# Kernel optimization log

Hardware: AMD Instinct MI355X
Metric: run time of the kernel (lower is better)

The kernel has to match this reference:

```python
import jax, jax.numpy as jnp
import numpy as np

D_MODEL = 512
NHEAD = 8
HEAD_DIM = D_MODEL // NHEAD  # 64
ROTARY_DIM = HEAD_DIM        # rotary_dim defaults to head_dim
WINDOW = (127, 128)          # (left, right) sliding window, flash-attn convention
ROPE_BASE = 10000.0


def setup_inputs() -> dict:
    key = jax.random.key(0)
    k1, k2, k3, k4 = jax.random.split(key, 4)
    N, T = 4, 2048
    x = jax.random.normal(k1, (N, T, D_MODEL), dtype=jnp.float32)
    # Wqkv: Linear(d_model, 3*d_model, bias=False) -> weight [3*D, D]
    Wqkv_w = jax.random.normal(k2, (3 * D_MODEL, D_MODEL), dtype=jnp.float32) * (D_MODEL ** -0.5)
    # out_proj: Linear(d_model, d_model, bias=True)
    out_w = jax.random.normal(k3, (D_MODEL, D_MODEL), dtype=jnp.float32) * (D_MODEL ** -0.5)
    out_b = jax.random.normal(k4, (D_MODEL,), dtype=jnp.float32) * 0.01
    return {"x": x, "Wqkv_w": Wqkv_w, "out_w": out_w, "out_b": out_b}


def _rope_cos_sin(T, dtype):
    # flash-attn RotaryEmbedding: inv_freq over even indices of rotary_dim
    inv_freq = 1.0 / (ROPE_BASE ** (jnp.arange(0, ROTARY_DIM, 2, dtype=jnp.float32) / ROTARY_DIM))
    t = jnp.arange(T, dtype=jnp.float32)
    freqs = jnp.outer(t, inv_freq)  # [T, ROTARY_DIM//2]
    return jnp.cos(freqs).astype(dtype), jnp.sin(freqs).astype(dtype)


def _apply_rotary(x, cos, sin):
    # non-interleaved (rotate halves); x: [N, T, H, hd], rotary over first ROTARY_DIM dims
    r, rest = x[..., :ROTARY_DIM], x[..., ROTARY_DIM:]
    half = ROTARY_DIM // 2
    x1, x2 = r[..., :half], r[..., half:]
    c = cos[None, :, None, :]  # [1, T, 1, half]
    s = sin[None, :, None, :]
    rotated = jnp.concatenate([x1 * c - x2 * s, x2 * c + x1 * s], axis=-1)
    return jnp.concatenate([rotated, rest], axis=-1) if rest.shape[-1] else rotated


def reference(x, Wqkv_w, out_w, out_b):
    N, T, D = x.shape
    qkv = jnp.einsum('ntd,ed->nte', x, Wqkv_w).reshape(N, T, 3, NHEAD, HEAD_DIM)
    q, k, v = qkv[:, :, 0], qkv[:, :, 1], qkv[:, :, 2]  # each [N, T, H, hd]
    cos, sin = _rope_cos_sin(T, x.dtype)
    q = _apply_rotary(q, cos, sin)
    k = _apply_rotary(k, cos, sin)
    scale = HEAD_DIM ** -0.5
    scores = jnp.einsum('nthd,nshd->nhts', q, k) * scale  # [N, H, T, T]
    # sliding window: query i attends key j iff i - left <= j <= i + right
    i = jnp.arange(T)[:, None]
    j = jnp.arange(T)[None, :]
    mask = (j >= i - WINDOW[0]) & (j <= i + WINDOW[1])  # [T, T]
    scores = jnp.where(mask[None, None], scores, jnp.finfo(scores.dtype).min)
    attn = jax.nn.softmax(scores, axis=-1)
    ctx = jnp.einsum('nhts,nshd->nthd', attn, v).reshape(N, T, D)
    return jnp.einsum('ntd,ed->nte', ctx, out_w) + out_b
```

## Files before the change

kernel.cpp:

```cpp
#include <hip/hip_runtime.h>
#include <math.h>

#define TSEQ 2048
#define NB 4
#define DM 512
#define NH 8
#define HD 64

typedef _Float16 half8 __attribute__((ext_vector_type(8)));
typedef _Float16 half4 __attribute__((ext_vector_type(4)));
typedef float floatx4 __attribute__((ext_vector_type(4)));

#if __has_builtin(__builtin_amdgcn_exp2f)
#define EXP2F(x) __builtin_amdgcn_exp2f(x)
#else
#define EXP2F(x) exp2f(x)
#endif

__device__ __forceinline__ void gl2lds16(const _Float16* g, _Float16* l) {
  const __attribute__((address_space(1))) unsigned int* gp =
      (const __attribute__((address_space(1))) unsigned int*)(uintptr_t)g;
  __attribute__((address_space(3))) unsigned int* lp =
      (__attribute__((address_space(3))) unsigned int*)(uintptr_t)l;
  __builtin_amdgcn_global_load_lds(gp, lp, 16, 0, 0);
}


__device__ __forceinline__ void cvt8(const float* __restrict__ src, char* __restrict__ dst,
                                     int unit_src, int unit_dst) {
  const float4 a = ((const float4*)src)[2 * unit_src];
  const float4 b = ((const float4*)src)[2 * unit_src + 1];
  half8 h;
  h[0] = (_Float16)a.x; h[1] = (_Float16)a.y; h[2] = (_Float16)a.z; h[3] = (_Float16)a.w;
  h[4] = (_Float16)b.x; h[5] = (_Float16)b.y; h[6] = (_Float16)b.z; h[7] = (_Float16)b.w;
  *(half8*)(dst + (size_t)unit_dst * 16) = h;
}

__global__ void prep(const float* __restrict__ x, const float* __restrict__ wqkv,
                     const float* __restrict__ ow, char* __restrict__ ws) {
  const int i = blockIdx.x * 256 + threadIdx.x;
  if (i < 524288) {
    cvt8(x, ws, i, i);
  } else if (i < 622592) {
    const int o = i - 524288;
    cvt8(wqkv, ws + 8650752, o, o);
  } else if (i < 655360) {
    const int o = i - 622592;
    cvt8(ow, ws + 10485760, o, o);
  } else {
    const int u = i - 655360;
    float4 o4;
    {
      const int id = 2 * u, t = id >> 5, fi = id & 31;
      const float invf = powf(10000.0f, -(float)(2 * fi) * (1.0f / 64.0f));
      float s, c; sincosf((float)t * invf, &s, &c);
      o4.x = c; o4.y = s;
    }
    {
      const int id = 2 * u + 1, t = id >> 5, fi = id & 31;
      const float invf = powf(10000.0f, -(float)(2 * fi) * (1.0f / 64.0f));
      float s, c; sincosf((float)t * invf, &s, &c);
      o4.z = c; o4.w = s;
    }
    ((float4*)(ws + 46137344))[u] = o4;
  }
}

__global__ __launch_bounds__(256) void qkv_gemm_mfma(
    const _Float16* __restrict__ A, const _Float16* __restrict__ B,
    const float2* __restrict__ rope,
    _Float16* __restrict__ qb, _Float16* __restrict__ kb, _Float16* __restrict__ vT)
{
  __shared__ __align__(16) _Float16 As0[128 * 32];
  __shared__ __align__(16) _Float16 Bs0[128 * 32];
  __shared__ __align__(16) _Float16 As1[128 * 32];
  __shared__ __align__(16) _Float16 Bs1[128 * 32];
  const int tid = threadIdx.x;
  const int wv = tid >> 6, lane = tid & 63, quad = lane >> 4, col = lane & 15;
  const int wm = wv >> 1, we = wv & 1;
  const int m0 = blockIdx.x << 7, c0 = blockIdx.y << 7;
  const int r0 = tid >> 2, p0 = tid & 3;
  const int cA0 = (p0 - (r0 >> 1)) & 3;
  const int r1 = (tid + 256) >> 2, p1 = tid & 3;
  const int cA1 = (p1 - (r1 >> 1)) & 3;
  const _Float16* ga0 = &A[(size_t)(m0 + r0) * DM + cA0 * 8];
  const _Float16* ga1 = &A[(size_t)(m0 + r1) * DM + cA1 * 8];
  const _Float16* gb0 = &B[(size_t)(c0 + r0) * DM + cA0 * 8];
  const _Float16* gb1 = &B[(size_t)(c0 + r1) * DM + cA1 * 8];
  floatx4 acc[4][4] = {};

#define QKV_STAGE(AS, BS, K)                      \
  do {                                            \
    gl2lds16(ga0 + (K), &AS[tid * 8]);            \
    gl2lds16(ga1 + (K), &AS[(tid + 256) * 8]);    \
    gl2lds16(gb0 + (K), &BS[tid * 8]);            \
    gl2lds16(gb1 + (K), &BS[(tid + 256) * 8]);    \
  } while (0)

#define QKV_COMPUTE(AS, BS)                                                   \
  do {                                                                        \
    half8 af[4], bf[4];                                                       \
    _Pragma("unroll") for (int mt = 0; mt < 4; mt++) {                        \
      const int R = wm * 64 + mt * 16 + col;                                  \
      af[mt] = *(const half8*)&AS[R * 32 + (((quad + (R >> 1)) & 3) << 3)];   \
    }                                                                         \
    _Pragma("unroll") for (int et = 0; et < 4; et++) {                        \
      const int R = we * 64 + et * 16 + col;                                  \
      bf[et] = *(const half8*)&BS[R * 32 + (((quad + (R >> 1)) & 3) << 3)];   \
    }                                                                         \
    _Pragma("unroll") for (int mt = 0; mt < 4; mt++)                          \
      _Pragma("unroll") for (int et = 0; et < 4; et++)                        \
        acc[mt][et] =                                                         \
            __builtin_amdgcn_mfma_f32_16x16x32_f16(af[mt], bf[et], acc[mt][et], 0, 0, 0); \
  } while (0)

  QKV_STAGE(As0, Bs0, 0);
  for (int k0 = 0; k0 < DM; k0 += 64) {
    __syncthreads();
    QKV_STAGE(As1, Bs1, k0 + 32);
    QKV_COMPUTE(As0, Bs0);
    __syncthreads();
    if (k0 + 64 < DM) QKV_STAGE(As0, Bs0, k0 + 64);
    QKV_COMPUTE(As1, Bs1);
  }
#undef QKV_STAGE
#undef QKV_COMPUTE

  const int eidx = (c0 >> 6) + we;
  const int three = eidx >> 3, h = eidx & 7;
  const int mbase = m0 + wm * 64 + quad * 4;
  if (three == 2) {
#pragma unroll
    for (int mt = 0; mt < 4; mt++) {
      const int m = mbase + mt * 16;
      const int n = m >> 11, t = m & 2047;
#pragma unroll
      for (int et = 0; et < 4; et++) {
        const int dh = et * 16 + col;
        half4 hv;
#pragma unroll
        for (int r = 0; r < 4; r++) hv[r] = (_Float16)acc[mt][et][r];
        *(half4*)&vT[(size_t)(n * NH + h) * HD * TSEQ + (size_t)dh * TSEQ + t] = hv;
      }
    }
  } else {
    _Float16* dst = three ? kb : qb;
    const float scl = three ? 1.0f : 0.125f * 1.4426950408889634f;
#pragma unroll
    for (int mt = 0; mt < 4; mt++)
#pragma unroll
      for (int r = 0; r < 4; r++) {
        const int m = mbase + mt * 16 + r;
        const int n = m >> 11, t = m & 2047;
#pragma unroll
        for (int et = 0; et < 4; et++) {
          const int i = ((et & 1) << 4) + col;
          const float2 cs = rope[t * 32 + i];
          const float v = acc[mt][et][r];
          const float v2 = acc[mt][et ^ 2][r];
          const float o = (et < 2) ? (v * cs.x - v2 * cs.y) : (v * cs.x + v2 * cs.y);
          dst[((size_t)(n * NH + h) * TSEQ + t) * HD + et * 16 + col] = (_Float16)(o * scl);
        }
      }
  }
}

__global__ __launch_bounds__(256, 4) void attn_win_mfma(
    const _Float16* __restrict__ qb, const _Float16* __restrict__ kb,
    const _Float16* __restrict__ vT, _Float16* __restrict__ ctx)
{
  __shared__ __align__(16) char smem[36864];
  _Float16* Ks = (_Float16*)smem;
  _Float16* Vt = (_Float16*)(smem + 9216);
  _Float16* Ps = (_Float16*)(smem + 18432);
  _Float16* Osh = (_Float16*)(smem + 27648);

  const int tid = threadIdx.x;
  const int wv = tid >> 6;
  const int lane = tid & 63;
  const int quad = lane >> 4;
  const int col = lane & 15;
  const int lin = (blockIdx.y << 5) | blockIdx.x;
  const int sl  = ((lin & 7) << 7) | (lin >> 3);
  const int nh = sl >> 5;
  const int q0 = (sl & 31) << 6;
  const _Float16* qp = qb + (size_t)nh * TSEQ * HD;
  const _Float16* kp = kb + (size_t)nh * TSEQ * HD;
  const _Float16* vp = vT + (size_t)nh * HD * TSEQ;

  const int i_row = (wv << 4) + col;
  const int ig = q0 + i_row;
  const half8 qf0 = *(const half8*)&qp[(size_t)ig * HD + (quad << 3)];
  const half8 qf1 = *(const half8*)&qp[(size_t)ig * HD + 32 + (quad << 3)];

  float l_i = 0.0f;
  floatx4 accO[4] = {};

  const int kt0 = max(0, q0 - 127) >> 6;
  const int kt1 = min(TSEQ - 1, q0 + 191) >> 6;
  const int kr = tid >> 2, kc = (tid & 3) << 4;
  const int vd = tid >> 2, vc = (tid & 3) << 4;
  const _Float16* kpr = kp + (size_t)kr * HD + kc;
  const _Float16* vpr = vp + (size_t)vd * TSEQ + vc;

  half8 ck0 = *(const half8*)(kpr + (size_t)(kt0 << 6) * HD);
  half8 ck1 = *(const half8*)(kpr + (size_t)(kt0 << 6) * HD + 8);
  half8 cv0 = *(const half8*)(vpr + (kt0 << 6));
  half8 cv1 = *(const half8*)(vpr + (kt0 << 6) + 8);

  for (int kt = kt0; kt <= kt1; kt++) {
    const int j0 = kt << 6;
    __syncthreads();
    *(half8*)&Ks[kr * 72 + kc] = ck0;
    *(half8*)&Ks[kr * 72 + kc + 8] = ck1;
    *(half8*)&Vt[vd * 72 + vc] = cv0;
    *(half8*)&Vt[vd * 72 + vc + 8] = cv1;
    __syncthreads();

    {
      const int jn = (kt < kt1) ? (j0 + 64) : j0;
      ck0 = *(const half8*)(kpr + (size_t)jn * HD);
      ck1 = *(const half8*)(kpr + (size_t)jn * HD + 8);
      cv0 = *(const half8*)(vpr + jn);
      cv1 = *(const half8*)(vpr + jn + 8);
    }

    floatx4 S[4];
#pragma unroll
    for (int js = 0; js < 4; js++) {
      const half8 a0 = *(const half8*)&Ks[((js << 4) + col) * 72 + (quad << 3)];
      const half8 a1 = *(const half8*)&Ks[((js << 4) + col) * 72 + 32 + (quad << 3)];
      floatx4 c = {0.f, 0.f, 0.f, 0.f};
      c = __builtin_amdgcn_mfma_f32_16x16x32_f16(a0, qf0, c, 0, 0, 0);
      c = __builtin_amdgcn_mfma_f32_16x16x32_f16(a1, qf1, c, 0, 0, 0);
      S[js] = c;
    }
    const int relb = j0 - ig + 127 + (quad << 2);
#pragma unroll
    for (int js = 0; js < 4; js++) {
      half4 ph;
#pragma unroll
      for (int r = 0; r < 4; r++) {
        const bool valid = (unsigned)(relb + (js << 4) + r) < 256u;
        const float p = valid ? EXP2F(S[js][r]) : 0.0f;
        l_i += p;
        ph[r] = (_Float16)p;
      }
      *(half4*)&Ps[i_row * 72 + (js << 4) + (quad << 2)] = ph;
    }
    const half8 pa0 = *(const half8*)&Ps[i_row * 72 + (quad << 3)];
    const half8 pa1 = *(const half8*)&Ps[i_row * 72 + 32 + (quad << 3)];
#pragma unroll
    for (int d4 = 0; d4 < 4; d4++) {
      const half8 vb0 = *(const half8*)&Vt[((d4 << 4) + col) * 72 + (quad << 3)];
      const half8 vb1 = *(const half8*)&Vt[((d4 << 4) + col) * 72 + 32 + (quad << 3)];
      accO[d4] = __builtin_amdgcn_mfma_f32_16x16x32_f16(pa0, vb0, accO[d4], 0, 0, 0);
      accO[d4] = __builtin_amdgcn_mfma_f32_16x16x32_f16(pa1, vb1, accO[d4], 0, 0, 0);
    }
  }
  l_i += __shfl_xor(l_i, 16, 64);
  l_i += __shfl_xor(l_i, 32, 64);
  {
    const float linv = 1.0f / l_i;
    float l4[4];
#pragma unroll
    for (int r = 0; r < 4; r++) l4[r] = __shfl(linv, (quad << 2) + r, 64);
#pragma unroll
    for (int d4 = 0; d4 < 4; d4++)
#pragma unroll
      for (int r = 0; r < 4; r++)
        Osh[((wv << 4) + (quad << 2) + r) * 72 + (d4 << 4) + col] = (_Float16)(accO[d4][r] * l4[r]);
  }
  __syncthreads();
  {
    const int n = nh >> 3, h = nh & 7;
    const int oi = tid >> 2, oc = (tid & 3) << 4;
    _Float16* dst = &ctx[((size_t)n * TSEQ + q0 + oi) * DM + h * HD + oc];
    *(half8*)&dst[0] = *(const half8*)&Osh[oi * 72 + oc];
    *(half8*)&dst[8] = *(const half8*)&Osh[oi * 72 + oc + 8];
  }
}

__global__ __launch_bounds__(256) void out_gemm_mfma(
    const _Float16* __restrict__ A, const _Float16* __restrict__ B,
    const float* __restrict__ bias, float* __restrict__ out)
{
  __shared__ _Float16 As[128 * 40];
  __shared__ _Float16 Bs[64 * 40];
  const int tid = threadIdx.x;
  const int wv = tid >> 6, lane = tid & 63, quad = lane >> 4, col = lane & 15;
  const int wm = wv >> 1, we = wv & 1;
  const int m0 = blockIdx.x << 7, c0 = blockIdx.y << 6;
  const int sr = tid >> 1, sc = (tid & 1) << 4;
  const int br = tid >> 2, bc = (tid & 3) << 3;
  const _Float16* ap = &A[(size_t)(m0 + sr) * DM + sc];
  const _Float16* bp = &B[(size_t)(c0 + br) * DM + bc];
  floatx4 acc[4][2] = {};
  half8 a0 = *(const half8*)(ap);
  half8 a1 = *(const half8*)(ap + 8);
  half8 b0 = *(const half8*)(bp);
  for (int k0 = 0; k0 < DM; k0 += 32) {
    __syncthreads();
    *(half8*)&As[sr * 40 + sc] = a0;
    *(half8*)&As[sr * 40 + sc + 8] = a1;
    *(half8*)&Bs[br * 40 + bc] = b0;
    half8 an0, an1, bn0;
    const bool more = (k0 + 32 < DM);
    if (more) {
      an0 = *(const half8*)(ap + k0 + 32);
      an1 = *(const half8*)(ap + k0 + 40);
      bn0 = *(const half8*)(bp + k0 + 32);
    }
    __syncthreads();
    half8 af[4], bf[2];
#pragma unroll
    for (int mt = 0; mt < 4; mt++)
      af[mt] = *(const half8*)&As[(wm * 64 + mt * 16 + col) * 40 + quad * 8];
#pragma unroll
    for (int et = 0; et < 2; et++)
      bf[et] = *(const half8*)&Bs[(we * 32 + et * 16 + col) * 40 + quad * 8];
#pragma unroll
    for (int mt = 0; mt < 4; mt++)
#pragma unroll
      for (int et = 0; et < 2; et++)
        acc[mt][et] = __builtin_amdgcn_mfma_f32_16x16x32_f16(af[mt], bf[et], acc[mt][et], 0, 0, 0);
    if (more) { a0 = an0; a1 = an1; b0 = bn0; }
  }
  float bb[2];
#pragma unroll
  for (int et = 0; et < 2; et++) bb[et] = bias[c0 + we * 32 + et * 16 + col];
  const int mbase = m0 + wm * 64 + quad * 4;
#pragma unroll
  for (int mt = 0; mt < 4; mt++)
#pragma unroll
    for (int r = 0; r < 4; r++) {
      const int m = mbase + mt * 16 + r;
#pragma unroll
      for (int et = 0; et < 2; et++)
        out[(size_t)m * DM + c0 + we * 32 + et * 16 + col] = acc[mt][et][r] + bb[et];
    }
}

extern "C" void kernel_launch(void* const* d_in, const int* in_sizes, int n_in,
                              void* d_out, int out_size, void* d_ws, size_t ws_size,
                              hipStream_t stream) {
  const float* x    = (const float*)d_in[0];
  const float* wqkv = (const float*)d_in[1];
  const float* ow   = (const float*)d_in[2];
  const float* ob   = (const float*)d_in[3];
  char* ws = (char*)d_ws;
  _Float16* xh    = (_Float16*)(ws);
  _Float16* wqkvh = (_Float16*)(ws + 8650752);
  _Float16* owh   = (_Float16*)(ws + 10485760);
  _Float16* qbuf  = (_Float16*)(ws + 11534336);
  _Float16* kbuf  = (_Float16*)(ws + 20971520);
  _Float16* vTb   = (_Float16*)(ws + 29360128);
  _Float16* ctxh  = (_Float16*)(ws + 37748736);
  float2*   rope  = (float2*)  (ws + 46137344);

  prep<<<2688, 256, 0, stream>>>(x, wqkv, ow, ws);
  qkv_gemm_mfma<<<dim3(64, 12), 256, 0, stream>>>(xh, wqkvh, rope, qbuf, kbuf, vTb);
  attn_win_mfma<<<dim3(32, 32), 256, 0, stream>>>(qbuf, kbuf, vTb, ctxh);
  out_gemm_mfma<<<dim3(64, 8), 256, 0, stream>>>(ctxh, owh, ob, (float*)d_out);
}
```

Before: 123.5 us.

## Skip out-of-window score subtiles and double-buffer out-proj GEMM via direct LDS loads

The attention loop now skips the QK MFMA and exp for 16-key subtiles that lie entirely outside each wave's sliding window, writing zero probabilities instead. The output projection GEMM switches to two LDS buffers filled with asynchronous global-to-LDS loads, using an XOR-style swizzle in place of padding. This aims to cut wasted matrix work at window edges and overlap global loads with MFMA compute. The asynchronous loads depend on barriers for completion, and the added branches can add divergence overhead.

```diff
diff --git a/kernel.cpp b/kernel.cpp
--- a/kernel.cpp
+++ b/kernel.cpp
@@ -202,6 +202,7 @@
   const int vd = tid >> 2, vc = (tid & 3) << 4;
   const _Float16* kpr = kp + (size_t)kr * HD + kc;
   const _Float16* vpr = vp + (size_t)vd * TSEQ + vc;
+  const int iw0 = q0 + (wv << 4);
 
   half8 ck0 = *(const half8*)(kpr + (size_t)(kt0 << 6) * HD);
   half8 ck1 = *(const half8*)(kpr + (size_t)(kt0 << 6) * HD + 8);
@@ -228,25 +229,34 @@
     floatx4 S[4];
 #pragma unroll
     for (int js = 0; js < 4; js++) {
-      const half8 a0 = *(const half8*)&Ks[((js << 4) + col) * 72 + (quad << 3)];
-      const half8 a1 = *(const half8*)&Ks[((js << 4) + col) * 72 + 32 + (quad << 3)];
-      floatx4 c = {0.f, 0.f, 0.f, 0.f};
-      c = __builtin_amdgcn_mfma_f32_16x16x32_f16(a0, qf0, c, 0, 0, 0);
-      c = __builtin_amdgcn_mfma_f32_16x16x32_f16(a1, qf1, c, 0, 0, 0);
-      S[js] = c;
+      const int jlo = j0 + (js << 4);
+      if ((unsigned)(jlo - iw0 + 142) < 286u) {
+        const half8 a0 = *(const half8*)&Ks[((js << 4) + col) * 72 + (quad << 3)];
+        const half8 a1 = *(const half8*)&Ks[((js << 4) + col) * 72 + 32 + (quad << 3)];
+        floatx4 c = {0.f, 0.f, 0.f, 0.f};
+        c = __builtin_amdgcn_mfma_f32_16x16x32_f16(a0, qf0, c, 0, 0, 0);
+        c = __builtin_amdgcn_mfma_f32_16x16x32_f16(a1, qf1, c, 0, 0, 0);
+        S[js] = c;
+      }
     }
     const int relb = j0 - ig + 127 + (quad << 2);
 #pragma unroll
     for (int js = 0; js < 4; js++) {
-      half4 ph;
-#pragma unroll
-      for (int r = 0; r < 4; r++) {
-        const bool valid = (unsigned)(relb + (js << 4) + r) < 256u;
-        const float p = valid ? EXP2F(S[js][r]) : 0.0f;
-        l_i += p;
-        ph[r] = (_Float16)p;
+      const int jlo = j0 + (js << 4);
+      if ((unsigned)(jlo - iw0 + 142) < 286u) {
+        half4 ph;
+#pragma unroll
+        for (int r = 0; r < 4; r++) {
+          const bool valid = (unsigned)(relb + (js << 4) + r) < 256u;
+          const float p = valid ? EXP2F(S[js][r]) : 0.0f;
+          l_i += p;
+          ph[r] = (_Float16)p;
+        }
+        *(half4*)&Ps[i_row * 72 + (js << 4) + (quad << 2)] = ph;
+      } else {
+        const half4 zz = {(_Float16)0.f, (_Float16)0.f, (_Float16)0.f, (_Float16)0.f};
+        *(half4*)&Ps[i_row * 72 + (js << 4) + (quad << 2)] = zz;
       }
-      *(half4*)&Ps[i_row * 72 + (js << 4) + (quad << 2)] = ph;
     }
     const half8 pa0 = *(const half8*)&Ps[i_row * 72 + (quad << 3)];
     const half8 pa1 = *(const half8*)&Ps[i_row * 72 + 32 + (quad << 3)];
@@ -285,47 +295,59 @@
     const _Float16* __restrict__ A, const _Float16* __restrict__ B,
     const float* __restrict__ bias, float* __restrict__ out)
 {
-  __shared__ _Float16 As[128 * 40];
-  __shared__ _Float16 Bs[64 * 40];
+  __shared__ __align__(16) _Float16 As0[128 * 32];
+  __shared__ __align__(16) _Float16 Bs0[64 * 32];
+  __shared__ __align__(16) _Float16 As1[128 * 32];
+  __shared__ __align__(16) _Float16 Bs1[64 * 32];
   const int tid = threadIdx.x;
   const int wv = tid >> 6, lane = tid & 63, quad = lane >> 4, col = lane & 15;
   const int wm = wv >> 1, we = wv & 1;
   const int m0 = blockIdx.x << 7, c0 = blockIdx.y << 6;
-  const int sr = tid >> 1, sc = (tid & 1) << 4;
-  const int br = tid >> 2, bc = (tid & 3) << 3;
-  const _Float16* ap = &A[(size_t)(m0 + sr) * DM + sc];
-  const _Float16* bp = &B[(size_t)(c0 + br) * DM + bc];
+  const int r0 = tid >> 2, p0 = tid & 3;
+  const int cA0 = (p0 - (r0 >> 1)) & 3;
+  const int r1 = (tid + 256) >> 2;
+  const int cA1 = (p0 - (r1 >> 1)) & 3;
+  const _Float16* ga0 = &A[(size_t)(m0 + r0) * DM + cA0 * 8];
+  const _Float16* ga1 = &A[(size_t)(m0 + r1) * DM + cA1 * 8];
+  const _Float16* gb0 = &B[(size_t)(c0 + r0) * DM + cA0 * 8];
   floatx4 acc[4][2] = {};
-  half8 a0 = *(const half8*)(ap);
-  half8 a1 = *(const half8*)(ap + 8);
-  half8 b0 = *(const half8*)(bp);
-  for (int k0 = 0; k0 < DM; k0 += 32) {
-    __syncthreads();
-    *(half8*)&As[sr * 40 + sc] = a0;
-    *(half8*)&As[sr * 40 + sc + 8] = a1;
-    *(half8*)&Bs[br * 40 + bc] = b0;
-    half8 an0, an1, bn0;
-    const bool more = (k0 + 32 < DM);
-    if (more) {
-      an0 = *(const half8*)(ap + k0 + 32);
-      an1 = *(const half8*)(ap + k0 + 40);
-      bn0 = *(const half8*)(bp + k0 + 32);
-    }
-    __syncthreads();
-    half8 af[4], bf[2];
-#pragma unroll
-    for (int mt = 0; mt < 4; mt++)
-      af[mt] = *(const half8*)&As[(wm * 64 + mt * 16 + col) * 40 + quad * 8];
-#pragma unroll
-    for (int et = 0; et < 2; et++)
-      bf[et] = *(const half8*)&Bs[(we * 32 + et * 16 + col) * 40 + quad * 8];
-#pragma unroll
-    for (int mt = 0; mt < 4; mt++)
-#pragma unroll
-      for (int et = 0; et < 2; et++)
-        acc[mt][et] = __builtin_amdgcn_mfma_f32_16x16x32_f16(af[mt], bf[et], acc[mt][et], 0, 0, 0);
-    if (more) { a0 = an0; a1 = an1; b0 = bn0; }
-  }
+
+#define OG_STAGE(AS, BS, K)                       \
+  do {                                            \
+    gl2lds16(ga0 + (K), &AS[tid * 8]);            \
+    gl2lds16(ga1 + (K), &AS[(tid + 256) * 8]);    \
+    gl2lds16(gb0 + (K), &BS[tid * 8]);            \
+  } while (0)
+
+#define OG_COMPUTE(AS, BS)                                                    \
+  do {                                                                        \
+    half8 af[4], bf[2];                                                       \
+    _Pragma("unroll") for (int mt = 0; mt < 4; mt++) {                        \
+      const int R = wm * 64 + mt * 16 + col;                                  \
+      af[mt] = *(const half8*)&AS[R * 32 + (((quad + (R >> 1)) & 3) << 3)];   \
+    }                                                                         \
+    _Pragma("unroll") for (int et = 0; et < 2; et++) {                        \
+      const int R = we * 32 + et * 16 + col;                                  \
+      bf[et] = *(const half8*)&BS[R * 32 + (((quad + (R >> 1)) & 3) << 3)];   \
+    }                                                                         \
+    _Pragma("unroll") for (int mt = 0; mt < 4; mt++)                          \
+      _Pragma("unroll") for (int et = 0; et < 2; et++)                        \
+        acc[mt][et] =                                                         \
+            __builtin_amdgcn_mfma_f32_16x16x32_f16(af[mt], bf[et], acc[mt][et], 0, 0, 0); \
+  } while (0)
+
+  OG_STAGE(As0, Bs0, 0);
+  for (int k0 = 0; k0 < DM; k0 += 64) {
+    __syncthreads();
+    OG_STAGE(As1, Bs1, k0 + 32);
+    OG_COMPUTE(As0, Bs0);
+    __syncthreads();
+    if (k0 + 64 < DM) OG_STAGE(As0, Bs0, k0 + 64);
+    OG_COMPUTE(As1, Bs1);
+  }
+#undef OG_STAGE
+#undef OG_COMPUTE
+
   float bb[2];
 #pragma unroll
   for (int et = 0; et < 2; et++) bb[et] = bias[c0 + we * 32 + et * 16 + col];
```

New measurement: 122.4 us. Within noise of the previous version (-0.9%).
